# Optimization experiments

Hardware: AMD Instinct MI355X
Metric: run time of the kernel (lower is better)

The kernel has to match this reference:

```python
import jax, jax.numpy as jnp
import numpy as np

D_EMBED = 768
N_HEADS = 12
HEAD_DIM = D_EMBED // N_HEADS


def setup_inputs() -> dict:
    key = jax.random.key(0)
    ks = jax.random.split(key, 9)
    B, T, C = 4, 2048, D_EMBED
    s = 1.0 / np.sqrt(C)
    return {
        "x": jax.random.normal(ks[0], (B, T, C), dtype=jnp.float32),
        "Wq": jax.random.normal(ks[1], (C, C), dtype=jnp.float32) * s,
        "bq": jnp.zeros((C,), dtype=jnp.float32),
        "Wk": jax.random.normal(ks[2], (C, C), dtype=jnp.float32) * s,
        "bk": jnp.zeros((C,), dtype=jnp.float32),
        "Wv": jax.random.normal(ks[3], (C, C), dtype=jnp.float32) * s,
        "bv": jnp.zeros((C,), dtype=jnp.float32),
        "Wo": jax.random.normal(ks[4], (C, C), dtype=jnp.float32) * s,
        "bo": jnp.zeros((C,), dtype=jnp.float32),
    }


def reference(x, Wq, bq, Wk, bk, Wv, bv, Wo, bo):
    B, T, C = x.shape
    H, D = N_HEADS, HEAD_DIM
    # projections -> [B, H, T, D]
    q = (x @ Wq + bq).reshape(B, T, H, D).transpose(0, 2, 1, 3)
    k = (x @ Wk + bk).reshape(B, T, H, D).transpose(0, 2, 1, 3)
    v = (x @ Wv + bv).reshape(B, T, H, D).transpose(0, 2, 1, 3)
    # full attention matrix [B, H, T, T] (faithful to manual implementation)
    scores = jnp.einsum('bhqd,bhkd->bhqk', q, k) / jnp.sqrt(jnp.float32(D))
    causal = jnp.tril(jnp.ones((T, T), dtype=bool))
    scores = jnp.where(causal, scores, jnp.float32(-jnp.inf))
    weights = jax.nn.softmax(scores, axis=-1)
    out = jnp.einsum('bhqk,bhkd->bhqd', weights, v)
    out = out.transpose(0, 2, 1, 3).reshape(B, T, C)
    return out @ Wo + bo
```

## Files before the change

kernel.cpp:

```cpp
#include <hip/hip_runtime.h>

#define T_LEN 2048
#define C_DIM 768
#define NH 12
#define HD 64
#define B_SZ 4
#define M_ROWS (B_SZ * T_LEN)
#define WSZ (C_DIM * C_DIM)
#define CH 520

typedef __bf16 bf16x8 __attribute__((ext_vector_type(8)));
typedef float f32x4 __attribute__((ext_vector_type(4)));
typedef float f32x16 __attribute__((ext_vector_type(16)));

__device__ __forceinline__ unsigned short f2bf(float f) {
    union { __bf16 b; unsigned short u; } c;
    c.b = (__bf16)f;
    return c.u;
}

__device__ __forceinline__ float fast_exp2(float x) {
    float r;
    asm("v_exp_f32 %0, %1" : "=v"(r) : "v"(x));
    return r;
}

__device__ __forceinline__ unsigned cvt_pk_bf16(float a, float b) {
    unsigned r;
    asm("v_cvt_pk_bf16_f32 %0, %1, %2" : "=v"(r) : "v"(a), "v"(b));
    return r;
}

__device__ __forceinline__ void perml32_swap(unsigned& a, unsigned& b) {
    asm("v_permlane32_swap_b32 %0, %1" : "+v"(a), "+v"(b));
}

__device__ __forceinline__ void gl2lds16(const void* g, void* l) {
    __builtin_amdgcn_global_load_lds(
        (const __attribute__((address_space(1))) unsigned int*)g,
        (__attribute__((address_space(3))) unsigned int*)l, 16, 0, 0);
}

__global__ __launch_bounds__(256) void conv_x(const float* __restrict__ x,
                                              unsigned short* __restrict__ xb)
{
    const int i = blockIdx.x * 256 + threadIdx.x;
    float4 v = ((const float4*)x)[i];
    ushort4 o;
    o.x = f2bf(v.x); o.y = f2bf(v.y); o.z = f2bf(v.z); o.w = f2bf(v.w);
    ((ushort4*)xb)[i] = o;
}

__global__ __launch_bounds__(256) void conv_wt(
    const float* __restrict__ W0, const float* __restrict__ W1,
    const float* __restrict__ W2, const float* __restrict__ W3,
    unsigned short* __restrict__ WtAll)
{
    __shared__ float tile[32][33];
    const int z = blockIdx.z;
    const float* W = (z == 0) ? W0 : (z == 1) ? W1 : (z == 2) ? W2 : W3;
    unsigned short* out = WtAll + (size_t)z * WSZ;
    const int k0 = blockIdx.x * 32, n0 = blockIdx.y * 32;
    const int r = threadIdx.x >> 3, c4 = (threadIdx.x & 7) * 4;
    float4 v = *(const float4*)&W[(size_t)(k0 + r) * C_DIM + n0 + c4];
    tile[r][c4 + 0] = v.x;
    tile[r][c4 + 1] = v.y;
    tile[r][c4 + 2] = v.z;
    tile[r][c4 + 3] = v.w;
    __syncthreads();
    ushort4 o;
    o.x = f2bf(tile[c4 + 0][r]);
    o.y = f2bf(tile[c4 + 1][r]);
    o.z = f2bf(tile[c4 + 2][r]);
    o.w = f2bf(tile[c4 + 3][r]);
    *(ushort4*)&out[(size_t)(n0 + r) * C_DIM + k0 + c4] = o;
}

__global__ __launch_bounds__(256) void gemm_bf16(
    const unsigned short* __restrict__ A, const unsigned short* __restrict__ WtAll,
    const float* __restrict__ b0, const float* __restrict__ b1,
    const float* __restrict__ b2,
    unsigned short* __restrict__ qg, unsigned short* __restrict__ kg,
    unsigned short* __restrict__ vtg, float* __restrict__ outF, int mode)
{
    __shared__ __align__(16) unsigned short As[2][8 * 512];
    __shared__ __align__(16) unsigned short Bs[2][8 * 512];
    const int tid = threadIdx.x;
    const int lane = tid & 63, w = tid >> 6;
    const int L15 = lane & 15, quad = lane >> 4;
    const int m0 = blockIdx.x * 128, n0 = blockIdx.y * 128;
    const int z = blockIdx.z;
    const unsigned short* W = WtAll + (size_t)z * WSZ;

    const int c0 = 2 * w, c1 = 2 * w + 1;
    const size_t aOff0 = (size_t)(m0 + c0 * 16 + L15) * C_DIM + quad * 8;
    const size_t aOff1 = (size_t)(m0 + c1 * 16 + L15) * C_DIM + quad * 8;
    const size_t bOff0 = (size_t)(n0 + c0 * 16 + L15) * C_DIM + quad * 8;
    const size_t bOff1 = (size_t)(n0 + c1 * 16 + L15) * C_DIM + quad * 8;

    f32x4 acc[4][4];
#pragma unroll
    for (int i = 0; i < 4; i++)
#pragma unroll
        for (int j = 0; j < 4; j++) acc[i][j] = 0.0f;

    const int cm = (w >> 1) * 4, cn = (w & 1) * 4;

    gl2lds16(&A[aOff0], &As[0][c0 * 512]);
    gl2lds16(&A[aOff1], &As[0][c1 * 512]);
    gl2lds16(&W[bOff0], &Bs[0][c0 * 512]);
    gl2lds16(&W[bOff1], &Bs[0][c1 * 512]);
    __syncthreads();

    for (int kt = 0; kt < 24; kt++) {
        const int cur = kt & 1;
        if (kt < 23) {
            const size_t o = (size_t)(kt + 1) * 32;
            gl2lds16(&A[aOff0 + o], &As[cur ^ 1][c0 * 512]);
            gl2lds16(&A[aOff1 + o], &As[cur ^ 1][c1 * 512]);
            gl2lds16(&W[bOff0 + o], &Bs[cur ^ 1][c0 * 512]);
            gl2lds16(&W[bOff1 + o], &Bs[cur ^ 1][c1 * 512]);
        }
        bf16x8 aF[4], bF[4];
#pragma unroll
        for (int i = 0; i < 4; i++)
            aF[i] = *(const bf16x8*)&As[cur][(cm + i) * 512 + lane * 8];
#pragma unroll
        for (int j = 0; j < 4; j++)
            bF[j] = *(const bf16x8*)&Bs[cur][(cn + j) * 512 + lane * 8];
#pragma unroll
        for (int i = 0; i < 4; i++)
#pragma unroll
            for (int j = 0; j < 4; j++)
                acc[i][j] = __builtin_amdgcn_mfma_f32_16x16x32_bf16(
                    aF[i], bF[j], acc[i][j], 0, 0, 0);
        __syncthreads();
    }

    const float* bias = (mode == 0) ? ((z == 0) ? b0 : (z == 1) ? b1 : b2) : b0;
    const float qscale = (z == 0 && mode == 0) ? 0.18033688011112042f : 1.0f;
#pragma unroll
    for (int i = 0; i < 4; i++) {
        const int mBase = m0 + (w >> 1) * 64 + i * 16 + quad * 4;
#pragma unroll
        for (int j = 0; j < 4; j++) {
            const int n = n0 + (w & 1) * 64 + j * 16 + L15;
            const float bn = bias[n];
            if (mode == 0) {
                const int h = n >> 6, d = n & 63;
                const int b = mBase >> 11, tB = mBase & (T_LEN - 1);
                if (z < 2) {
                    unsigned short* o = (z == 0) ? qg : kg;
#pragma unroll
                    for (int r = 0; r < 4; r++)
                        o[(((size_t)(b * NH + h)) * T_LEN + tB + r) * HD + d] =
                            f2bf((acc[i][j][r] + bn) * qscale);
                } else {
                    ushort4 o4;
                    o4.x = f2bf(acc[i][j][0] + bn);
                    o4.y = f2bf(acc[i][j][1] + bn);
                    o4.z = f2bf(acc[i][j][2] + bn);
                    o4.w = f2bf(acc[i][j][3] + bn);
                    *(ushort4*)&vtg[(((size_t)(b * NH + h)) * HD + d) * T_LEN + tB] = o4;
                }
            } else {
#pragma unroll
                for (int r = 0; r < 4; r++)
                    outF[(size_t)(mBase + r) * C_DIM + n] = acc[i][j][r] + bn;
            }
        }
    }
}

__global__ __launch_bounds__(256, 4) void attn_mfma(
    const unsigned short* __restrict__ qg, const unsigned short* __restrict__ kg,
    const unsigned short* __restrict__ vtg, unsigned short* __restrict__ attb)
{
    __shared__ __align__(16) unsigned short Ks[2][8 * CH];
    __shared__ __align__(16) unsigned short Vs[2][8 * CH];
    const int tid = threadIdx.x;
    const int lane = tid & 63, w = tid >> 6;
    const int L15 = lane & 15, L31 = lane & 31;
    const int quad = lane >> 4, r4 = (lane >> 4) & 1, r5 = lane >> 5;

    const int n = blockIdx.x;
    const int bh = n % (B_SZ * NH);
    const int m = n / (B_SZ * NH);
    const int qi = (m & 1) ? (m >> 1) : (15 - (m >> 1));
    const size_t base = (size_t)bh * T_LEN * HD;
    const int q0 = qi * 128;
    const int nk = 2 * qi + 2;
    const int qrow = q0 + w * 32 + L31;

    bf16x8 qf[4];
#pragma unroll
    for (int kc = 0; kc < 4; kc++)
        qf[kc] = *(const bf16x8*)&qg[base + (size_t)qrow * HD + kc * 16 + r5 * 8];

    f32x16 accO[2];
#pragma unroll
    for (int md = 0; md < 2; md++) accO[md] = 0.0f;
    f32x4 lacc = 0.0f;

    auto stage = [&](int kt, int buf) {
        const int ktb = kt * 64;
        gl2lds16(&kg[base + (size_t)(ktb + w * 16 + L15) * HD + quad * 8],
                 &Ks[buf][(2 * w) * CH]);
        gl2lds16(&kg[base + (size_t)(ktb + w * 16 + L15) * HD + 32 + quad * 8],
                 &Ks[buf][(2 * w + 1) * CH]);
        gl2lds16(&vtg[base + (size_t)(w * 16 + L15) * T_LEN + ktb + quad * 8],
                 &Vs[buf][(2 * w) * CH]);
        gl2lds16(&vtg[base + (size_t)(w * 16 + L15) * T_LEN + ktb + 32 + quad * 8],
                 &Vs[buf][(2 * w + 1) * CH]);
    };

    stage(0, 0);
    __syncthreads();

    const int qmaxw = q0 + w * 32 + 31;
    const int qminw = q0 + w * 32;

    for (int kt = 0; kt < nk; kt++) {
        const int cur = kt & 1;
        if (kt + 1 < nk) stage(kt + 1, cur ^ 1);
        const int ktb = kt * 64;
        if (ktb <= qmaxw) {
            f32x16 sa[2];
#pragma unroll
            for (int mi = 0; mi < 2; mi++) {
                sa[mi] = 0.0f;
#pragma unroll
                for (int kc = 0; kc < 4; kc++) {
                    const int ck = mi * 4 + r4 * 2 + (kc >> 1);
                    const int slot = L15 + 16 * ((kc & 1) * 2 + r5);
                    bf16x8 kf = *(const bf16x8*)&Ks[cur][ck * CH + slot * 8];
                    sa[mi] = __builtin_amdgcn_mfma_f32_32x32x16_bf16(
                        kf, qf[kc], sa[mi], 0, 0, 0);
                }
            }
            const bool needmask = (ktb + 63 > qminw);
            bf16x8 pfrag[4];
#pragma unroll
            for (int mi = 0; mi < 2; mi++) {
                float e[16];
#pragma unroll
                for (int g = 0; g < 4; g++) {
#pragma unroll
                    for (int rr = 0; rr < 4; rr++) {
                        float s = sa[mi][g * 4 + rr];
                        if (needmask) {
                            const int key = ktb + mi * 32 + 8 * g + 4 * r5 + rr;
                            s = (key <= qrow) ? s : -1e30f;
                        }
                        e[g * 4 + rr] = fast_exp2(s);
                        lacc[rr] += e[g * 4 + rr];
                    }
                }
#pragma unroll
                for (int h = 0; h < 2; h++) {
                    unsigned a0 = cvt_pk_bf16(e[8 * h + 0], e[8 * h + 1]);
                    unsigned a1 = cvt_pk_bf16(e[8 * h + 2], e[8 * h + 3]);
                    unsigned b0 = cvt_pk_bf16(e[8 * h + 4], e[8 * h + 5]);
                    unsigned b1 = cvt_pk_bf16(e[8 * h + 6], e[8 * h + 7]);
                    perml32_swap(a0, b0);
                    perml32_swap(a1, b1);
                    union { unsigned u[4]; bf16x8 v; } pf;
                    pf.u[0] = a0; pf.u[1] = a1; pf.u[2] = b0; pf.u[3] = b1;
                    pfrag[2 * mi + h] = pf.v;
                }
            }
#pragma unroll
            for (int md = 0; md < 2; md++) {
#pragma unroll
                for (int kc = 0; kc < 4; kc++) {
                    const int cv = md * 4 + r4 * 2 + (kc >> 1);
                    const int slot = L15 + 16 * ((kc & 1) * 2 + r5);
                    bf16x8 vf = *(const bf16x8*)&Vs[cur][cv * CH + slot * 8];
                    accO[md] = __builtin_amdgcn_mfma_f32_32x32x16_bf16(
                        vf, pfrag[kc], accO[md], 0, 0, 0);
                }
            }
        }
        __syncthreads();
    }

    const float l = (lacc[0] + lacc[1]) + (lacc[2] + lacc[3]);
    const float lt = l + __shfl_xor(l, 32, 64);
    const float inv = __builtin_amdgcn_rcpf(lt);
    const int b = bh / NH, h = bh % NH;
    const size_t orow = ((size_t)(b * T_LEN + qrow)) * C_DIM + h * HD;
#pragma unroll
    for (int md = 0; md < 2; md++) {
#pragma unroll
        for (int g = 0; g < 4; g++) {
            uint2 wv;
            wv.x = (unsigned)f2bf(accO[md][g * 4 + 0] * inv) |
                   ((unsigned)f2bf(accO[md][g * 4 + 1] * inv) << 16);
            wv.y = (unsigned)f2bf(accO[md][g * 4 + 2] * inv) |
                   ((unsigned)f2bf(accO[md][g * 4 + 3] * inv) << 16);
            *(uint2*)&attb[orow + md * 32 + 8 * g + 4 * r5] = wv;
        }
    }
}

extern "C" void kernel_launch(void* const* d_in, const int* in_sizes, int n_in,
                              void* d_out, int out_size, void* d_ws, size_t ws_size,
                              hipStream_t stream)
{
    const float* x  = (const float*)d_in[0];
    const float* Wq = (const float*)d_in[1];
    const float* bq = (const float*)d_in[2];
    const float* Wk = (const float*)d_in[3];
    const float* bk = (const float*)d_in[4];
    const float* Wv = (const float*)d_in[5];
    const float* bv = (const float*)d_in[6];
    const float* Wo = (const float*)d_in[7];
    const float* bo = (const float*)d_in[8];
    float* out = (float*)d_out;

    const size_t nMC = (size_t)M_ROWS * C_DIM;
    unsigned short* xb   = (unsigned short*)d_ws;
    unsigned short* Wt   = xb + nMC;
    unsigned short* qg   = Wt + 4 * (size_t)WSZ;
    unsigned short* kg   = qg + nMC;
    unsigned short* vtg  = kg + nMC;
    unsigned short* attb = vtg + nMC;

    conv_x<<<(int)(nMC / 1024), 256, 0, stream>>>(x, xb);
    conv_wt<<<dim3(24, 24, 4), 256, 0, stream>>>(Wq, Wk, Wv, Wo, Wt);
    gemm_bf16<<<dim3(64, 6, 3), 256, 0, stream>>>(xb, Wt, bq, bk, bv,
                                                  qg, kg, vtg, nullptr, 0);
    attn_mfma<<<16 * B_SZ * NH, 256, 0, stream>>>(qg, kg, vtg, attb);
    gemm_bf16<<<dim3(64, 6, 1), 256, 0, stream>>>(attb, Wt + 3 * (size_t)WSZ,
                                                  bo, bo, bo, nullptr, nullptr,
                                                  nullptr, out, 1);
}
```

Measured before the change: 249.4 us.

## Add dedicated 256x256-tile QKV GEMM kernel with swizzled LDS and block remap

Replaces the generic QKV projection launch with a new kernel that uses 512 threads and 256x256 output tiles over the concatenated Wq/Wk/Wv weights. It adds XOR-swizzled LDS layouts, a grouped block-index remap for L2 locality, and split fragment loads interleaved with MFMA phases using barriers and setprio. The aim is higher arithmetic intensity and better MFMA utilisation in the projection. In exchange it uses more LDS and registers per block and launches only 288 blocks, which may leave some CUs idle. The output GEMM is reduced to a simpler single-purpose kernel.

New measurement: 247.5 us. About the same (-0.8%).

```diff
diff --git a/kernel.cpp b/kernel.cpp
--- a/kernel.cpp
+++ b/kernel.cpp
@@ -76,12 +76,177 @@
     *(ushort4*)&out[(size_t)(n0 + r) * C_DIM + k0 + c4] = o;
 }
 
-__global__ __launch_bounds__(256) void gemm_bf16(
-    const unsigned short* __restrict__ A, const unsigned short* __restrict__ WtAll,
+__global__ __launch_bounds__(512, 2) void gemm_qkv(
+    const unsigned short* __restrict__ A, const unsigned short* __restrict__ Wt,
     const float* __restrict__ b0, const float* __restrict__ b1,
     const float* __restrict__ b2,
     unsigned short* __restrict__ qg, unsigned short* __restrict__ kg,
-    unsigned short* __restrict__ vtg, float* __restrict__ outF, int mode)
+    unsigned short* __restrict__ vtg)
+{
+    __shared__ __align__(16) unsigned short As[2][256 * 64];
+    __shared__ __align__(16) unsigned short Bs[2][256 * 64];
+
+    const int tid = threadIdx.x;
+    const int lane = tid & 63, w = tid >> 6;
+    const int L15 = lane & 15, quad = lane >> 4;
+    const int wm = w >> 2, wn = w & 3;
+
+    const int raw = blockIdx.x;
+    const int swz = (raw & 7) * 36 + (raw >> 3);
+    const int mx = swz & 31;
+    const int ny = swz >> 5;
+
+    const int lr = lane >> 3;
+    const int lg = (lane & 7) ^ lr;
+    const size_t aRow0 = (size_t)(mx * 256 + w * 8 + lr) * C_DIM + lg * 8;
+    const size_t bRow0 = (size_t)(ny * 256 + w * 8 + lr) * C_DIM + lg * 8;
+
+    const int sg0 = ((quad) ^ (L15 & 7)) * 16;
+    const int sg1 = ((4 + quad) ^ (L15 & 7)) * 16;
+    const int aRowB = (wm * 128 + L15) * 128;
+    const int bRowB = (wn * 64 + L15) * 128;
+
+    f32x4 acc[8][4];
+#pragma unroll
+    for (int i = 0; i < 8; i++)
+#pragma unroll
+        for (int j = 0; j < 4; j++) acc[i][j] = 0.0f;
+
+#pragma unroll
+    for (int i = 0; i < 4; i++) {
+        gl2lds16(&A[aRow0 + (size_t)i * (64 * C_DIM)], &As[0][(i * 8 + w) * 512]);
+        gl2lds16(&Wt[bRow0 + (size_t)i * (64 * C_DIM)], &Bs[0][(i * 8 + w) * 512]);
+    }
+    __syncthreads();
+
+    for (int kt = 0; kt < 12; kt++) {
+        const int cur = kt & 1;
+        const char* Ac = (const char*)(cur ? As[1] : As[0]);
+        const char* Bc = (const char*)(cur ? Bs[1] : Bs[0]);
+        bf16x8 av[4][2], bL[2][2], bH[2][2];
+
+#pragma unroll
+        for (int fr = 0; fr < 4; fr++)
+#pragma unroll
+            for (int kh = 0; kh < 2; kh++)
+                av[fr][kh] = *(const bf16x8*)(Ac + aRowB + fr * 2048 + (kh ? sg1 : sg0));
+#pragma unroll
+        for (int fc = 0; fc < 2; fc++)
+#pragma unroll
+            for (int kh = 0; kh < 2; kh++)
+                bL[fc][kh] = *(const bf16x8*)(Bc + bRowB + fc * 2048 + (kh ? sg1 : sg0));
+        if (kt < 11) {
+            const size_t ko = (size_t)(kt + 1) * 64;
+#pragma unroll
+            for (int i = 0; i < 4; i++) {
+                gl2lds16(&A[aRow0 + (size_t)i * (64 * C_DIM) + ko],
+                         &As[cur ^ 1][(i * 8 + w) * 512]);
+                gl2lds16(&Wt[bRow0 + (size_t)i * (64 * C_DIM) + ko],
+                         &Bs[cur ^ 1][(i * 8 + w) * 512]);
+            }
+        }
+        __builtin_amdgcn_s_barrier();
+        asm volatile("s_waitcnt lgkmcnt(0)" ::: "memory");
+        __builtin_amdgcn_sched_barrier(0);
+        __builtin_amdgcn_s_setprio(1);
+#pragma unroll
+        for (int fr = 0; fr < 4; fr++)
+#pragma unroll
+            for (int fc = 0; fc < 2; fc++)
+#pragma unroll
+                for (int kh = 0; kh < 2; kh++)
+                    acc[fr][fc] = __builtin_amdgcn_mfma_f32_16x16x32_bf16(
+                        av[fr][kh], bL[fc][kh], acc[fr][fc], 0, 0, 0);
+        __builtin_amdgcn_s_setprio(0);
+        __builtin_amdgcn_s_barrier();
+
+#pragma unroll
+        for (int fc = 0; fc < 2; fc++)
+#pragma unroll
+            for (int kh = 0; kh < 2; kh++)
+                bH[fc][kh] = *(const bf16x8*)(Bc + bRowB + (fc + 2) * 2048 + (kh ? sg1 : sg0));
+        __builtin_amdgcn_s_barrier();
+        asm volatile("s_waitcnt lgkmcnt(0)" ::: "memory");
+        __builtin_amdgcn_sched_barrier(0);
+        __builtin_amdgcn_s_setprio(1);
+#pragma unroll
+        for (int fr = 0; fr < 4; fr++)
+#pragma unroll
+            for (int fc = 0; fc < 2; fc++)
+#pragma unroll
+                for (int kh = 0; kh < 2; kh++)
+                    acc[fr][fc + 2] = __builtin_amdgcn_mfma_f32_16x16x32_bf16(
+                        av[fr][kh], bH[fc][kh], acc[fr][fc + 2], 0, 0, 0);
+        __builtin_amdgcn_s_setprio(0);
+        __builtin_amdgcn_s_barrier();
+
+#pragma unroll
+        for (int fr = 0; fr < 4; fr++)
+#pragma unroll
+            for (int kh = 0; kh < 2; kh++)
+                av[fr][kh] = *(const bf16x8*)(Ac + aRowB + (fr + 4) * 2048 + (kh ? sg1 : sg0));
+        __builtin_amdgcn_s_barrier();
+        asm volatile("s_waitcnt lgkmcnt(0)" ::: "memory");
+        __builtin_amdgcn_sched_barrier(0);
+        __builtin_amdgcn_s_setprio(1);
+#pragma unroll
+        for (int fr = 0; fr < 4; fr++)
+#pragma unroll
+            for (int fc = 0; fc < 2; fc++)
+#pragma unroll
+                for (int kh = 0; kh < 2; kh++)
+                    acc[fr + 4][fc + 2] = __builtin_amdgcn_mfma_f32_16x16x32_bf16(
+                        av[fr][kh], bH[fc][kh], acc[fr + 4][fc + 2], 0, 0, 0);
+#pragma unroll
+        for (int fr = 0; fr < 4; fr++)
+#pragma unroll
+            for (int fc = 0; fc < 2; fc++)
+#pragma unroll
+                for (int kh = 0; kh < 2; kh++)
+                    acc[fr + 4][fc] = __builtin_amdgcn_mfma_f32_16x16x32_bf16(
+                        av[fr][kh], bL[fc][kh], acc[fr + 4][fc], 0, 0, 0);
+        __builtin_amdgcn_s_setprio(0);
+        asm volatile("s_waitcnt vmcnt(0)" ::: "memory");
+        __builtin_amdgcn_s_barrier();
+    }
+
+    const int z = ny / 3;
+    const float* bias = (z == 0) ? b0 : (z == 1) ? b1 : b2;
+    const float qs = (z == 0) ? 0.18033688011112042f : 1.0f;
+    const int mrow = mx * 256 + wm * 128;
+    const int ncol = ny * 256 + wn * 64;
+#pragma unroll
+    for (int fc = 0; fc < 4; fc++) {
+        const int n = ncol + fc * 16 + L15;
+        const int nl = n - z * 768;
+        const int h = nl >> 6, d = nl & 63;
+        const float bn = bias[nl];
+#pragma unroll
+        for (int fr = 0; fr < 8; fr++) {
+            const int mB = mrow + fr * 16 + quad * 4;
+            const int b = mB >> 11, tB = mB & (T_LEN - 1);
+            if (z < 2) {
+                unsigned short* o = z ? kg : qg;
+#pragma unroll
+                for (int r = 0; r < 4; r++)
+                    o[(((size_t)(b * NH + h)) * T_LEN + tB + r) * HD + d] =
+                        f2bf((acc[fr][fc][r] + bn) * qs);
+            } else {
+                ushort4 o4;
+                o4.x = f2bf(acc[fr][fc][0] + bn);
+                o4.y = f2bf(acc[fr][fc][1] + bn);
+                o4.z = f2bf(acc[fr][fc][2] + bn);
+                o4.w = f2bf(acc[fr][fc][3] + bn);
+                *(ushort4*)&vtg[(((size_t)(b * NH + h)) * HD + d) * T_LEN + tB] = o4;
+            }
+        }
+    }
+}
+
+__global__ __launch_bounds__(256) void gemm_bf16(
+    const unsigned short* __restrict__ A, const unsigned short* __restrict__ WtAll,
+    const float* __restrict__ b0,
+    float* __restrict__ outF)
 {
     __shared__ __align__(16) unsigned short As[2][8 * 512];
     __shared__ __align__(16) unsigned short Bs[2][8 * 512];
@@ -89,8 +254,7 @@
     const int lane = tid & 63, w = tid >> 6;
     const int L15 = lane & 15, quad = lane >> 4;
     const int m0 = blockIdx.x * 128, n0 = blockIdx.y * 128;
-    const int z = blockIdx.z;
-    const unsigned short* W = WtAll + (size_t)z * WSZ;
+    const unsigned short* W = WtAll;
 
     const int c0 = 2 * w, c1 = 2 * w + 1;
     const size_t aOff0 = (size_t)(m0 + c0 * 16 + L15) * C_DIM + quad * 8;
@@ -137,37 +301,16 @@
         __syncthreads();
     }
 
-    const float* bias = (mode == 0) ? ((z == 0) ? b0 : (z == 1) ? b1 : b2) : b0;
-    const float qscale = (z == 0 && mode == 0) ? 0.18033688011112042f : 1.0f;
 #pragma unroll
     for (int i = 0; i < 4; i++) {
         const int mBase = m0 + (w >> 1) * 64 + i * 16 + quad * 4;
 #pragma unroll
         for (int j = 0; j < 4; j++) {
             const int n = n0 + (w & 1) * 64 + j * 16 + L15;
-            const float bn = bias[n];
-            if (mode == 0) {
-                const int h = n >> 6, d = n & 63;
-                const int b = mBase >> 11, tB = mBase & (T_LEN - 1);
-                if (z < 2) {
-                    unsigned short* o = (z == 0) ? qg : kg;
-#pragma unroll
-                    for (int r = 0; r < 4; r++)
-                        o[(((size_t)(b * NH + h)) * T_LEN + tB + r) * HD + d] =
-                            f2bf((acc[i][j][r] + bn) * qscale);
-                } else {
-                    ushort4 o4;
-                    o4.x = f2bf(acc[i][j][0] + bn);
-                    o4.y = f2bf(acc[i][j][1] + bn);
-                    o4.z = f2bf(acc[i][j][2] + bn);
-                    o4.w = f2bf(acc[i][j][3] + bn);
-                    *(ushort4*)&vtg[(((size_t)(b * NH + h)) * HD + d) * T_LEN + tB] = o4;
-                }
-            } else {
-#pragma unroll
-                for (int r = 0; r < 4; r++)
-                    outF[(size_t)(mBase + r) * C_DIM + n] = acc[i][j][r] + bn;
-            }
+            const float bn = b0[n];
+#pragma unroll
+            for (int r = 0; r < 4; r++)
+                outF[(size_t)(mBase + r) * C_DIM + n] = acc[i][j][r] + bn;
         }
     }
 }
@@ -328,10 +471,8 @@
 
     conv_x<<<(int)(nMC / 1024), 256, 0, stream>>>(x, xb);
     conv_wt<<<dim3(24, 24, 4), 256, 0, stream>>>(Wq, Wk, Wv, Wo, Wt);
-    gemm_bf16<<<dim3(64, 6, 3), 256, 0, stream>>>(xb, Wt, bq, bk, bv,
-                                                  qg, kg, vtg, nullptr, 0);
+    gemm_qkv<<<288, 512, 0, stream>>>(xb, Wt, bq, bk, bv, qg, kg, vtg);
     attn_mfma<<<16 * B_SZ * NH, 256, 0, stream>>>(qg, kg, vtg, attb);
-    gemm_bf16<<<dim3(64, 6, 1), 256, 0, stream>>>(attb, Wt + 3 * (size_t)WSZ,
-                                                  bo, bo, bo, nullptr, nullptr,
-                                                  nullptr, out, 1);
-}
+    gemm_bf16<<<dim3(64, 6), 256, 0, stream>>>(attb, Wt + 3 * (size_t)WSZ,
+                                               bo, out);
+}
```

## Rewrite projection GEMMs with BK=64, swizzled LDS, XCD-aware tile mapping

Applied to the files above, without the earlier changes.

Replaces the generic GEMM with a templated kernel that uses a K-step of 64 with an XOR-swizzled LDS layout to reduce bank conflicts. Non-square N tiles are used: 192 for the fused QKV projection, treated as one 2304-wide GEMM, and 96 for the output projection. Block indices are remapped so that tiles sharing A rows land on the same XCD for L2 reuse. MFMA priority raising and halving the number of barriers aim to improve MFMA utilisation. In exchange, each block uses more LDS and registers, which may limit occupancy, and the QKV boundaries must line up with the tiles (768 is divisible by 192).

Measured after the change: 213.0 us. 1.17x faster.

```diff
diff --git a/kernel.cpp b/kernel.cpp
--- a/kernel.cpp
+++ b/kernel.cpp
@@ -76,97 +76,130 @@
     *(ushort4*)&out[(size_t)(n0 + r) * C_DIM + k0 + c4] = o;
 }
 
-__global__ __launch_bounds__(256) void gemm_bf16(
-    const unsigned short* __restrict__ A, const unsigned short* __restrict__ WtAll,
+template <int BN, int MODE>
+__global__ __launch_bounds__(256, 2) void gemm_tile(
+    const unsigned short* __restrict__ A, const unsigned short* __restrict__ Wt,
     const float* __restrict__ b0, const float* __restrict__ b1,
     const float* __restrict__ b2,
     unsigned short* __restrict__ qg, unsigned short* __restrict__ kg,
-    unsigned short* __restrict__ vtg, float* __restrict__ outF, int mode)
-{
-    __shared__ __align__(16) unsigned short As[2][8 * 512];
-    __shared__ __align__(16) unsigned short Bs[2][8 * 512];
+    unsigned short* __restrict__ vtg, float* __restrict__ outF)
+{
+    constexpr int NFC = BN / 32;
+    constexpr int NY = (MODE == 0 ? 2304 : 768) / BN;
+    __shared__ __align__(16) unsigned short As[2][128 * 64];
+    __shared__ __align__(16) unsigned short Bs[2][BN * 64];
+
     const int tid = threadIdx.x;
     const int lane = tid & 63, w = tid >> 6;
     const int L15 = lane & 15, quad = lane >> 4;
-    const int m0 = blockIdx.x * 128, n0 = blockIdx.y * 128;
-    const int z = blockIdx.z;
-    const unsigned short* W = WtAll + (size_t)z * WSZ;
-
-    const int c0 = 2 * w, c1 = 2 * w + 1;
-    const size_t aOff0 = (size_t)(m0 + c0 * 16 + L15) * C_DIM + quad * 8;
-    const size_t aOff1 = (size_t)(m0 + c1 * 16 + L15) * C_DIM + quad * 8;
-    const size_t bOff0 = (size_t)(n0 + c0 * 16 + L15) * C_DIM + quad * 8;
-    const size_t bOff1 = (size_t)(n0 + c1 * 16 + L15) * C_DIM + quad * 8;
-
-    f32x4 acc[4][4];
-#pragma unroll
-    for (int i = 0; i < 4; i++)
-#pragma unroll
-        for (int j = 0; j < 4; j++) acc[i][j] = 0.0f;
-
-    const int cm = (w >> 1) * 4, cn = (w & 1) * 4;
-
-    gl2lds16(&A[aOff0], &As[0][c0 * 512]);
-    gl2lds16(&A[aOff1], &As[0][c1 * 512]);
-    gl2lds16(&W[bOff0], &Bs[0][c0 * 512]);
-    gl2lds16(&W[bOff1], &Bs[0][c1 * 512]);
+    const int wm = w >> 1, wn = w & 1;
+
+    const int raw = blockIdx.x;
+    const int xcd = raw & 7, i = raw >> 3;
+    const int mx = xcd * 8 + i / NY;
+    const int ny = i % NY;
+
+    const int lr = lane >> 3;
+    const int lg8 = (lane & 7) ^ lr;
+    const size_t aBase = (size_t)(mx * 128 + w * 8 + lr) * C_DIM + lg8 * 8;
+    const size_t bBase = (size_t)(ny * BN + w * 8 + lr) * C_DIM + lg8 * 8;
+
+    auto stage = [&](int kt, int buf) {
+        const size_t ko = (size_t)kt * 64;
+#pragma unroll
+        for (int c = 0; c < 4; c++)
+            gl2lds16(&A[aBase + (size_t)c * 32 * C_DIM + ko],
+                     &As[buf][(c * 32 + w * 8) * 64]);
+#pragma unroll
+        for (int c = 0; c < BN / 32; c++)
+            gl2lds16(&Wt[bBase + (size_t)c * 32 * C_DIM + ko],
+                     &Bs[buf][(c * 32 + w * 8) * 64]);
+    };
+
+    const int sg0 = (quad ^ (L15 & 7)) * 16;
+    const int sg1 = ((4 + quad) ^ (L15 & 7)) * 16;
+    const int aRowB = (wm * 64 + L15) * 128;
+    const int bRowB = (wn * (BN / 2) + L15) * 128;
+
+    f32x4 acc[4][NFC];
+#pragma unroll
+    for (int fr = 0; fr < 4; fr++)
+#pragma unroll
+        for (int fc = 0; fc < NFC; fc++) acc[fr][fc] = 0.0f;
+
+    stage(0, 0);
     __syncthreads();
 
-    for (int kt = 0; kt < 24; kt++) {
+    for (int kt = 0; kt < 12; kt++) {
         const int cur = kt & 1;
-        if (kt < 23) {
-            const size_t o = (size_t)(kt + 1) * 32;
-            gl2lds16(&A[aOff0 + o], &As[cur ^ 1][c0 * 512]);
-            gl2lds16(&A[aOff1 + o], &As[cur ^ 1][c1 * 512]);
-            gl2lds16(&W[bOff0 + o], &Bs[cur ^ 1][c0 * 512]);
-            gl2lds16(&W[bOff1 + o], &Bs[cur ^ 1][c1 * 512]);
-        }
-        bf16x8 aF[4], bF[4];
-#pragma unroll
-        for (int i = 0; i < 4; i++)
-            aF[i] = *(const bf16x8*)&As[cur][(cm + i) * 512 + lane * 8];
-#pragma unroll
-        for (int j = 0; j < 4; j++)
-            bF[j] = *(const bf16x8*)&Bs[cur][(cn + j) * 512 + lane * 8];
-#pragma unroll
-        for (int i = 0; i < 4; i++)
-#pragma unroll
-            for (int j = 0; j < 4; j++)
-                acc[i][j] = __builtin_amdgcn_mfma_f32_16x16x32_bf16(
-                    aF[i], bF[j], acc[i][j], 0, 0, 0);
+        if (kt < 11) stage(kt + 1, cur ^ 1);
+        const char* Ac = (const char*)As[cur];
+        const char* Bc = (const char*)Bs[cur];
+        bf16x8 av[4][2], bv[NFC][2];
+#pragma unroll
+        for (int fr = 0; fr < 4; fr++)
+#pragma unroll
+            for (int kh = 0; kh < 2; kh++)
+                av[fr][kh] = *(const bf16x8*)(Ac + aRowB + fr * 2048 + (kh ? sg1 : sg0));
+#pragma unroll
+        for (int fc = 0; fc < NFC; fc++)
+#pragma unroll
+            for (int kh = 0; kh < 2; kh++)
+                bv[fc][kh] = *(const bf16x8*)(Bc + bRowB + fc * 2048 + (kh ? sg1 : sg0));
+        __builtin_amdgcn_s_setprio(1);
+#pragma unroll
+        for (int fr = 0; fr < 4; fr++)
+#pragma unroll
+            for (int fc = 0; fc < NFC; fc++)
+#pragma unroll
+                for (int kh = 0; kh < 2; kh++)
+                    acc[fr][fc] = __builtin_amdgcn_mfma_f32_16x16x32_bf16(
+                        av[fr][kh], bv[fc][kh], acc[fr][fc], 0, 0, 0);
+        __builtin_amdgcn_s_setprio(0);
         __syncthreads();
     }
 
-    const float* bias = (mode == 0) ? ((z == 0) ? b0 : (z == 1) ? b1 : b2) : b0;
-    const float qscale = (z == 0 && mode == 0) ? 0.18033688011112042f : 1.0f;
-#pragma unroll
-    for (int i = 0; i < 4; i++) {
-        const int mBase = m0 + (w >> 1) * 64 + i * 16 + quad * 4;
-#pragma unroll
-        for (int j = 0; j < 4; j++) {
-            const int n = n0 + (w & 1) * 64 + j * 16 + L15;
-            const float bn = bias[n];
-            if (mode == 0) {
-                const int h = n >> 6, d = n & 63;
-                const int b = mBase >> 11, tB = mBase & (T_LEN - 1);
+    if (MODE == 0) {
+        const int z = (ny * BN) / 768;
+        const float* bias = (z == 0) ? b0 : (z == 1) ? b1 : b2;
+        const float qs = (z == 0) ? 0.18033688011112042f : 1.0f;
+#pragma unroll
+        for (int fc = 0; fc < NFC; fc++) {
+            const int n = ny * BN + wn * (BN / 2) + fc * 16 + L15;
+            const int nl = n - z * 768;
+            const int h = nl >> 6, d = nl & 63;
+            const float bn = bias[nl];
+#pragma unroll
+            for (int fr = 0; fr < 4; fr++) {
+                const int mB = mx * 128 + wm * 64 + fr * 16 + quad * 4;
+                const int b = mB >> 11, tB = mB & (T_LEN - 1);
                 if (z < 2) {
-                    unsigned short* o = (z == 0) ? qg : kg;
+                    unsigned short* o = z ? kg : qg;
 #pragma unroll
                     for (int r = 0; r < 4; r++)
                         o[(((size_t)(b * NH + h)) * T_LEN + tB + r) * HD + d] =
-                            f2bf((acc[i][j][r] + bn) * qscale);
+                            f2bf((acc[fr][fc][r] + bn) * qs);
                 } else {
                     ushort4 o4;
-                    o4.x = f2bf(acc[i][j][0] + bn);
-                    o4.y = f2bf(acc[i][j][1] + bn);
-                    o4.z = f2bf(acc[i][j][2] + bn);
-                    o4.w = f2bf(acc[i][j][3] + bn);
+                    o4.x = f2bf(acc[fr][fc][0] + bn);
+                    o4.y = f2bf(acc[fr][fc][1] + bn);
+                    o4.z = f2bf(acc[fr][fc][2] + bn);
+                    o4.w = f2bf(acc[fr][fc][3] + bn);
                     *(ushort4*)&vtg[(((size_t)(b * NH + h)) * HD + d) * T_LEN + tB] = o4;
                 }
-            } else {
+            }
+        }
+    } else {
+#pragma unroll
+        for (int fc = 0; fc < NFC; fc++) {
+            const int n = ny * BN + wn * (BN / 2) + fc * 16 + L15;
+            const float bn = b0[n];
+#pragma unroll
+            for (int fr = 0; fr < 4; fr++) {
+                const int mB = mx * 128 + wm * 64 + fr * 16 + quad * 4;
 #pragma unroll
                 for (int r = 0; r < 4; r++)
-                    outF[(size_t)(mBase + r) * C_DIM + n] = acc[i][j][r] + bn;
+                    outF[(size_t)(mB + r) * C_DIM + n] = acc[fr][fc][r] + bn;
             }
         }
     }
@@ -328,10 +361,10 @@
 
     conv_x<<<(int)(nMC / 1024), 256, 0, stream>>>(x, xb);
     conv_wt<<<dim3(24, 24, 4), 256, 0, stream>>>(Wq, Wk, Wv, Wo, Wt);
-    gemm_bf16<<<dim3(64, 6, 3), 256, 0, stream>>>(xb, Wt, bq, bk, bv,
-                                                  qg, kg, vtg, nullptr, 0);
+    gemm_tile<192, 0><<<768, 256, 0, stream>>>(xb, Wt, bq, bk, bv,
+                                               qg, kg, vtg, nullptr);
     attn_mfma<<<16 * B_SZ * NH, 256, 0, stream>>>(qg, kg, vtg, attb);
-    gemm_bf16<<<dim3(64, 6, 1), 256, 0, stream>>>(attb, Wt + 3 * (size_t)WSZ,
-                                                  bo, bo, bo, nullptr, nullptr,
-                                                  nullptr, out, 1);
-}
+    gemm_tile<96, 1><<<512, 256, 0, stream>>>(attb, Wt + 3 * (size_t)WSZ,
+                                              bo, bo, bo, nullptr, nullptr,
+                                              nullptr, out);
+}
```
